# Kernel tuning notes

Hardware: AMD Instinct MI355X
Metric: run time of the kernel (lower is better)

## Reference

```python
import jax, jax.numpy as jnp
import numpy as np

B, CIN, H, W = 2, 8, 224, 224
P, S, K, WIN = 10, 5, 7, 3      # patchsize, stride, k neighbours, window radius = 15 // stride
E, F = 8, 64                    # embedding out-channels, cnn hidden features
N1 = (H - P) // S + 1
N2 = (W - P) // S + 1
N = N1 * N2                     # patches per image (43*43 = 1849)


def _conv(x, w, b):
    y = jax.lax.conv_general_dilated(x, w, (1, 1), 'SAME',
                                     dimension_numbers=('NCHW', 'OIHW', 'NCHW'))
    return y + b[None, :, None, None]


def _cnn3(x, w1, b1, w2, b2, w3, b3):
    # conv-relu, conv-relu, conv (depth=3, bn disabled)
    h = jax.nn.relu(_conv(x, w1, b1))
    h = jax.nn.relu(_conv(h, w2, b2))
    return _conv(h, w3, b3)


def _patches(x):
    # x: [B,C,H,W] -> [B, N, C*P*P] (im2col with stride S)
    ri = jnp.arange(N1)[:, None] * S + jnp.arange(P)[None, :]   # [N1,P]
    ci = jnp.arange(N2)[:, None] * S + jnp.arange(P)[None, :]   # [N2,P]
    p = x[:, :, ri, :][..., ci]            # [B,C,N1,P,N2,P]
    p = p.transpose(0, 2, 4, 1, 3, 5)      # [B,N1,N2,C,P,P]
    return p.reshape(x.shape[0], N, -1)


def _candidates():
    q1, q2 = jnp.meshgrid(jnp.arange(N1), jnp.arange(N2), indexing='ij')
    off = jnp.arange(-WIN, WIN + 1)
    c1 = jnp.clip(q1[..., None, None] + off[:, None], 0, N1 - 1)   # [N1,N2,7,7]
    c2 = jnp.clip(q2[..., None, None] + off[None, :], 0, N2 - 1)
    return (c1 * N2 + c2).reshape(N, -1)   # [N, m], m=49


def _fold(pats, C):
    # pats: [B,N,C*P*P] -> [B,C,H,W], overlap-add then normalize by counts
    pats = pats.reshape(B, N, C, P, P).transpose(0, 2, 1, 3, 4).reshape(B, C, -1)
    rr = jnp.arange(N1)[:, None] * S + jnp.arange(P)[None, :]
    cc = jnp.arange(N2)[:, None] * S + jnp.arange(P)[None, :]
    R = jnp.broadcast_to(rr[:, None, :, None], (N1, N2, P, P)).reshape(-1)
    Cc = jnp.broadcast_to(cc[None, :, None, :], (N1, N2, P, P)).reshape(-1)
    out = jnp.zeros((B, C, H, W), pats.dtype).at[:, :, R, Cc].add(pats)
    cnt = jnp.zeros((H, W), pats.dtype).at[R, Cc].add(1.0)
    return out / jnp.maximum(cnt, 1.0)


def setup_inputs() -> dict:
    key = jax.random.key(0)
    ks = jax.random.split(key, 8)
    sd = 0.05
    d = {"x": jax.random.normal(ks[0], (B, CIN, H, W), jnp.float32)}
    # embedding cnn: CIN->F->F->E
    d["w1e"] = jax.random.normal(ks[1], (F, CIN, 3, 3), jnp.float32) * sd
    d["b1e"] = jnp.zeros((F,), jnp.float32)
    d["w2e"] = jax.random.normal(ks[2], (F, F, 3, 3), jnp.float32) * sd
    d["b2e"] = jnp.zeros((F,), jnp.float32)
    d["w3e"] = jax.random.normal(ks[3], (E, F, 3, 3), jnp.float32) * sd
    d["b3e"] = jnp.zeros((E,), jnp.float32)
    # temperature cnn: CIN->F->F->1
    d["w1t"] = jax.random.normal(ks[4], (F, CIN, 3, 3), jnp.float32) * sd
    d["b1t"] = jnp.zeros((F,), jnp.float32)
    d["w2t"] = jax.random.normal(ks[5], (F, F, 3, 3), jnp.float32) * sd
    d["b2t"] = jnp.zeros((F,), jnp.float32)
    d["w3t"] = jax.random.normal(ks[6], (1, F, 3, 3), jnp.float32) * sd
    d["b3t"] = jnp.zeros((1,), jnp.float32)
    return d


def reference(x, w1e, b1e, w2e, b2e, w3e, b3e, w1t, b1t, w2t, b2t, w3t, b3t):
    xe = _cnn3(x, w1e, b1e, w2e, b2e, w3e, b3e)           # [B,E,H,W] patch embedding
    log_temp = _cnn3(x, w1t, b1t, w2t, b2t, w3t, b3t)     # [B,1,H,W] log temperature

    pe = _patches(xe)                                     # [B,N,E*P*P]
    yp = _patches(x)                                      # [B,N,CIN*P*P]
    lt = _patches(log_temp).mean(-1)                      # [B,N] per-patch log temp
    idx = _candidates()                                   # [N,m]

    # negative squared euclidean distance, gathered at window candidates
    sq = jnp.sum(pe * pe, -1)                             # [B,N]
    G = jnp.einsum('bnd,bmd->bnm', pe, pe)                # [B,N,N] patch Gram
    Dfull = -(sq[:, :, None] + sq[:, None, :] - 2.0 * G)
    Dc = Dfull[:, jnp.arange(N)[:, None], idx]            # [B,N,m]

    self_mask = (idx == jnp.arange(N)[:, None])[None]     # exclude_self=True
    logits = Dc * jnp.exp(-lt)[..., None]                 # temperature-scaled
    logits = jnp.where(self_mask, -1e9, logits)

    # continuous (neural) k-nearest-neighbour weights
    ws, cur = [], logits
    for _ in range(K):
        w = jax.nn.softmax(cur, axis=-1)
        ws.append(w)
        cur = cur + jnp.log1p(-jnp.minimum(w, 1.0 - 1e-6))
    Wk = jnp.stack(ws, axis=-1)                           # [B,N,m,K]

    yg = yp[:, idx]                                       # [B,N,m,dy] gathered neighbour patches
    nb = jnp.einsum('bnmk,bnmd->kbnd', Wk, yg)            # [K,B,N,dy]
    vols = [_fold(nb[j], CIN) for j in range(K)]
    return jnp.concatenate([x] + vols, axis=1)            # [B,(K+1)*CIN,H,W]
```

## Files before the change

kernel.cpp:

```cpp
#include <hip/hip_runtime.h>
#include <math.h>

namespace {
constexpr int B_ = 2, CIN = 8, H_ = 224, W_ = 224;
constexpr int K_ = 7;
constexpr int F_ = 64, E_ = 8;
constexpr int N1 = 43, N2 = 43, N_ = N1 * N2;
constexpr int M_ = 49;
constexpr int D_ = 800;
constexpr int HW = H_ * W_;

constexpr size_t FHW = (size_t)B_ * F_ * HW;
constexpr size_t OFF_H1E = 0;
constexpr size_t OFF_H1T = OFF_H1E + FHW;
constexpr size_t OFF_H2E = OFF_H1T + FHW;
constexpr size_t OFF_H2T = OFF_H2E + FHW;
constexpr size_t OFF_WK  = 0;
constexpr size_t OFF_XCL = OFF_H1T;
constexpr size_t OFF_XE  = OFF_H2T + FHW;
constexpr size_t OFF_LTM = OFF_XE + (size_t)B_ * E_ * HW;
constexpr size_t OFF_PE  = OFF_LTM + (size_t)B_ * HW;
constexpr size_t OFF_LT  = OFF_PE + (size_t)B_ * N_ * D_;
constexpr size_t OFF_SQ  = OFF_LT + (size_t)B_ * N_;
constexpr int WPREP_N = 294912;
constexpr int WPREP1_N = 12288;
constexpr int WPREP3_N = 9216;
constexpr int WPREP_TOT = WPREP_N + WPREP1_N + 2 * WPREP3_N;

__device__ __forceinline__ int clampi(int v, int lo, int hi) {
  return min(max(v, lo), hi);
}

__device__ __forceinline__ int xcd_swz(int x, int nwg) {
  int xcd = x & 7, idx = x >> 3;
  int q = nwg >> 3, r = nwg & 7;
  int base = (xcd < r) ? xcd * (q + 1) : r * (q + 1) + (xcd - r) * q;
  return base + idx;
}

__device__ __forceinline__ unsigned short bf16_rne(float v) {
  unsigned u = __float_as_uint(v);
  return (unsigned short)((u + 0x7FFFu + ((u >> 16) & 1u)) >> 16);
}

typedef __attribute__((ext_vector_type(8))) short short8;
typedef __attribute__((ext_vector_type(4))) float float4v;
typedef __attribute__((ext_vector_type(2))) float float2v;
typedef __attribute__((ext_vector_type(4))) unsigned short ushort4v;
}

__global__ __launch_bounds__(256) void wprep_k(
    const float* __restrict__ w_e, const float* __restrict__ w_t,
    const float* __restrict__ w1e, const float* __restrict__ w1t,
    const float* __restrict__ w3e, const float* __restrict__ w3t,
    unsigned short* __restrict__ whi, unsigned short* __restrict__ wlo,
    unsigned short* __restrict__ whi1, unsigned short* __restrict__ wlo1,
    unsigned short* __restrict__ whi3, unsigned short* __restrict__ wlo3) {
  int t = blockIdx.x * 256 + threadIdx.x;
  if (t >= WPREP_TOT) return;
  float v;
  unsigned short* dh;
  unsigned short* dl;
  int di;
  if (t < WPREP_N) {
    int j = t & 7;
    int lane = (t >> 3) & 63;
    int wv = (t >> 9) & 3;
    int t2 = t >> 11;
    int idx = t2 % 9;
    int t3 = t2 / 9;
    int kcb = t3 & 1;
    int br = t3 >> 1;
    const float* wgt = br ? w_t : w_e;
    int co = wv * 16 + (lane & 15);
    int ci = kcb * 32 + 8 * (lane >> 4) + j;
    v = wgt[((size_t)co * 64 + ci) * 9 + idx];
    dh = whi; dl = wlo; di = t;
  } else if (t < WPREP_N + WPREP1_N) {
    int t1 = t - WPREP_N;
    int j = t1 & 7;
    int lane = (t1 >> 3) & 63;
    int wv = (t1 >> 9) & 3;
    int t2 = t1 >> 11;
    int ky = t2 % 3;
    int br = t2 / 3;
    const float* wgt = br ? w1t : w1e;
    int co = wv * 16 + (lane & 15);
    int kx = lane >> 4;
    int ci = j;
    v = (kx < 3) ? wgt[(((size_t)co * 8 + ci) * 3 + ky) * 3 + kx] : 0.f;
    dh = whi1; dl = wlo1; di = t1;
  } else {
    int t3v = t - WPREP_N - WPREP1_N;
    int set = t3v / WPREP3_N;
    int rem = t3v - set * WPREP3_N;
    int j = rem & 7;
    int lane = (rem >> 3) & 63;
    int t2 = rem >> 9;
    int idx = t2 % 9;
    int kcb = t2 / 9;
    int co = lane & 15;
    int ci = kcb * 32 + 8 * (lane >> 4) + j;
    if (set == 0)
      v = (co < 8) ? w3e[((size_t)co * 64 + ci) * 9 + idx] : 0.f;
    else
      v = (co == 0) ? w3t[(size_t)ci * 9 + idx] : 0.f;
    dh = whi3; dl = wlo3; di = t3v;
  }
  unsigned u = __float_as_uint(v);
  unsigned short hi = (unsigned short)(u >> 16);
  float rem = v - __uint_as_float(u & 0xffff0000u);
  unsigned short lo = (unsigned short)(__float_as_uint(rem) >> 16);
  dh[di] = hi;
  dl[di] = lo;
}

__global__ __launch_bounds__(256) void conv1_k(
    const float* __restrict__ x,
    const unsigned short* __restrict__ whi1, const unsigned short* __restrict__ wlo1,
    const float* __restrict__ b_e, unsigned short* __restrict__ o_e,
    const float* __restrict__ b_t, unsigned short* __restrict__ o_t) {
  const int tile = blockIdx.x;
  const int b = blockIdx.z & 1;
  const int br = blockIdx.z >> 1;
  const float* bias = br ? b_t : b_e;
  unsigned short* out = br ? o_t : o_e;

  const int th0 = (tile / 14) * 16, tw0 = (tile % 14) * 16;
  const int tid = threadIdx.x;
  const int wv = tid >> 6, lane = tid & 63;
  const int q = lane >> 4, n = lane & 15;

  __shared__ unsigned short sT[342 * 20];

  const float* xB = x + (size_t)b * CIN * HW;
#pragma unroll
  for (int it = 0; it < 2; ++it) {
    int s = tid + 256 * it;
    if (s < 342) {
      int lr = s / 19, lc = s - lr * 19;
      int gh = th0 + lr - 1, gw = tw0 + lc - 1;
      short8 h8, l8;
#pragma unroll
      for (int ci = 0; ci < 8; ++ci) { h8[ci] = 0; l8[ci] = 0; }
      if (lc < 18 && gh >= 0 && gh < H_ && gw >= 0 && gw < W_) {
        const float* xp = xB + (size_t)gh * W_ + gw;
#pragma unroll
        for (int ci = 0; ci < 8; ++ci) {
          float v = xp[(size_t)ci * HW];
          unsigned u = __float_as_uint(v);
          float rem = v - __uint_as_float(u & 0xffff0000u);
          h8[ci] = (short)(u >> 16);
          l8[ci] = (short)(__float_as_uint(rem) >> 16);
        }
      }
      *(short8*)&sT[s * 20] = h8;
      *(short8*)&sT[s * 20 + 8] = l8;
    }
  }

  const short8* wh8 = (const short8*)whi1;
  const short8* wl8 = (const short8*)wlo1;
  short8 Ah[3], Al[3];
#pragma unroll
  for (int ky = 0; ky < 3; ++ky) {
    int ab = ((br * 3 + ky) * 4 + wv) * 64 + lane;
    Ah[ky] = wh8[ab];
    Al[ky] = wl8[ab];
  }

  float4v acc[16];
#pragma unroll
  for (int pr = 0; pr < 16; ++pr) acc[pr] = (float4v)0.f;

  __syncthreads();

#pragma unroll
  for (int r = 0; r < 18; ++r) {
    const unsigned short* p = &sT[(r * 19 + n + q) * 20];
    short8 Bh = *(const short8*)p;
    short8 Bl = *(const short8*)(p + 8);
#pragma unroll
    for (int ky = 0; ky < 3; ++ky) {
      const int pr = r - ky;
      if (pr >= 0 && pr < 16) {
        acc[pr] = __builtin_amdgcn_mfma_f32_16x16x32_bf16(Ah[ky], Bh, acc[pr], 0, 0, 0);
        acc[pr] = __builtin_amdgcn_mfma_f32_16x16x32_bf16(Al[ky], Bh, acc[pr], 0, 0, 0);
        acc[pr] = __builtin_amdgcn_mfma_f32_16x16x32_bf16(Ah[ky], Bl, acc[pr], 0, 0, 0);
      }
    }
  }

  float4v bv = *(const float4v*)&bias[wv * 16 + 4 * q];
#pragma unroll
  for (int pr = 0; pr < 16; ++pr) {
    ushort4v hv;
#pragma unroll
    for (int r = 0; r < 4; ++r)
      hv[r] = bf16_rne(fmaxf(acc[pr][r] + bv[r], 0.f));
    *(ushort4v*)&out[(((size_t)b * H_ + th0 + pr) * W_ + tw0 + n) * 64 + wv * 16 + 4 * q] = hv;
  }
}

__global__ __launch_bounds__(256) void conv2_mfma_k(
    const unsigned short* __restrict__ in_e, const unsigned short* __restrict__ in_t,
    const unsigned short* __restrict__ whi, const unsigned short* __restrict__ wlo,
    const float* __restrict__ b_e, const float* __restrict__ b_t,
    unsigned short* __restrict__ ehi, unsigned short* __restrict__ elo,
    unsigned short* __restrict__ thi, unsigned short* __restrict__ tlo) {
  constexpr int NLD = 12;
  const int tile = blockIdx.x;
  const int b = blockIdx.z & 1;
  const int br = blockIdx.z >> 1;
  const unsigned short* in = br ? in_t : in_e;
  const float* bias = br ? b_t : b_e;
  unsigned short* ohi = br ? thi : ehi;
  unsigned short* olo = br ? tlo : elo;

  const int th0 = (tile / 14) * 8, tw0 = (tile % 14) * 16;
  const int tid = threadIdx.x;
  const int wv = tid >> 6, lane = tid & 63;
  const int q = lane >> 4, n = lane & 15;

  __shared__ unsigned short sT[2 * 128 * 68];
  unsigned* sT32 = (unsigned*)sT;

  float4v acc[8];
#pragma unroll
  for (int pr = 0; pr < 8; ++pr) acc[pr] = (float4v)0.f;

  const unsigned short* inB = in + (size_t)b * HW * 64;
  const short8* whi8 = (const short8*)whi;
  const short8* wlo8 = (const short8*)wlo;

  int po[NLD];
  unsigned okm = 0;
#pragma unroll
  for (int j = 0; j < NLD; ++j) {
    int s = tid + 256 * j;
    int sp = s >> 4, cp = s & 15;
    int lr = sp / 18, lc = sp - lr * 18;
    int gh = th0 + lr - 1, gw = tw0 + lc - 1;
    bool ok = (s < 2880) && gh >= 0 && gh < H_ && gw >= 0 && gw < W_;
    po[j] = ok ? (gh * W_ + gw) * 64 + 2 * cp : 0;
    if (ok) okm |= (1u << j);
  }

  for (int kcb = 0; kcb < 2; ++kcb) {
    unsigned stg[NLD];
#pragma unroll
    for (int j = 0; j < NLD; ++j)
      stg[j] = *(const unsigned*)&inB[(size_t)po[j] + kcb * 32];

    __syncthreads();
#pragma unroll
    for (int j = 0; j < NLD; ++j) {
      int s = tid + 256 * j;
      if (s < 2880) {
        int sp = s >> 4, cp = s & 15;
        sT32[sp * 18 + cp] = ((okm >> j) & 1) ? stg[j] : 0u;
      }
    }
    __syncthreads();

    short8 Ah[9], Al[9];
    const int abase = (((br * 2 + kcb) * 9) * 4 + wv) * 64 + lane;
#pragma unroll
    for (int idx = 0; idx < 9; ++idx) {
      Ah[idx] = whi8[abase + idx * 256];
      Al[idx] = wlo8[abase + idx * 256];
    }

#pragma unroll
    for (int r = 0; r < 10; ++r) {
      short8 Bh[3];
#pragma unroll
      for (int kx = 0; kx < 3; ++kx)
        Bh[kx] = *(const short8*)&sT[(r * 18 + n + kx) * 36 + 8 * q];
#pragma unroll
      for (int ky = 0; ky < 3; ++ky) {
        const int pr = r - ky;
        if (pr >= 0 && pr < 8) {
#pragma unroll
          for (int kx = 0; kx < 3; ++kx) {
            const int idx = ky * 3 + kx;
            acc[pr] = __builtin_amdgcn_mfma_f32_16x16x32_bf16(Ah[idx], Bh[kx], acc[pr], 0, 0, 0);
            acc[pr] = __builtin_amdgcn_mfma_f32_16x16x32_bf16(Al[idx], Bh[kx], acc[pr], 0, 0, 0);
          }
        }
      }
    }
  }

  float4v bv = *(const float4v*)&bias[wv * 16 + 4 * q];
  unsigned short* sHi = (unsigned short*)sT;
  unsigned short* sLo = sHi + 128 * 68;
  __syncthreads();
#pragma unroll
  for (int pr = 0; pr < 8; ++pr) {
    int px = pr * 16 + n;
    ushort4v hv, lv;
#pragma unroll
    for (int r = 0; r < 4; ++r) {
      float v = fmaxf(acc[pr][r] + bv[r], 0.f);
      unsigned u = __float_as_uint(v);
      float rem = v - __uint_as_float(u & 0xffff0000u);
      hv[r] = (unsigned short)(u >> 16);
      lv[r] = (unsigned short)(__float_as_uint(rem) >> 16);
    }
    *(ushort4v*)&sHi[px * 68 + wv * 16 + 4 * q] = hv;
    *(ushort4v*)&sLo[px * 68 + wv * 16 + 4 * q] = lv;
  }
  __syncthreads();
#pragma unroll
  for (int i = 0; i < 4; ++i) {
    int f = tid + 256 * i;
    int px = f >> 3, c8 = f & 7;
    int h = th0 + (px >> 4), w = tw0 + (px & 15);
    size_t o = ((size_t)(b * H_ + h) * W_ + w) * 64 + c8 * 8;
    *(short8*)&ohi[o] = *(const short8*)&sHi[px * 68 + c8 * 8];
    *(short8*)&olo[o] = *(const short8*)&sLo[px * 68 + c8 * 8];
  }
}

__global__ __launch_bounds__(256) void conv3_mfma_k(
    const unsigned short* __restrict__ h2ehi, const unsigned short* __restrict__ h2elo,
    const unsigned short* __restrict__ h2thi, const unsigned short* __restrict__ h2tlo,
    const unsigned short* __restrict__ whi3, const unsigned short* __restrict__ wlo3,
    const float* __restrict__ b3e, const float* __restrict__ b3t,
    float* __restrict__ xe, float* __restrict__ ltm) {
  constexpr int NLD = 12;
  const int tile = blockIdx.x;
  const int b = blockIdx.z & 1;
  const int br = blockIdx.z >> 1;
  const unsigned short* ihi = (br ? h2thi : h2ehi) + (size_t)b * HW * 64;
  const unsigned short* ilo = (br ? h2tlo : h2elo) + (size_t)b * HW * 64;

  const int th0 = (tile / 14) * 8, tw0 = (tile % 14) * 16;
  const int tid = threadIdx.x;
  const int wv = tid >> 6, lane = tid & 63;
  const int q = lane >> 4, n = lane & 15;

  __shared__ unsigned short sT[180 * 72];
  unsigned* sT32 = (unsigned*)sT;

  int po[NLD];
  unsigned okm = 0;
#pragma unroll
  for (int j = 0; j < NLD; ++j) {
    int s = tid + 256 * j;
    int sp = s >> 4, cp = s & 15;
    int lr = sp / 18, lc = sp - lr * 18;
    int gh = th0 + lr - 1, gw = tw0 + lc - 1;
    bool ok = (s < 2880) && gh >= 0 && gh < H_ && gw >= 0 && gw < W_;
    po[j] = ok ? (gh * W_ + gw) * 64 + 2 * cp : 0;
    if (ok) okm |= (1u << j);
  }

  const short8* wh8 = (const short8*)whi3;
  const short8* wl8 = (const short8*)wlo3;
  const int brBase = br * 1152;

  float4v acc[2];
  acc[0] = (float4v)0.f;
  acc[1] = (float4v)0.f;

  for (int kcb = 0; kcb < 2; ++kcb) {
    unsigned sgh[NLD], sgl[NLD];
#pragma unroll
    for (int j = 0; j < NLD; ++j) {
      sgh[j] = *(const unsigned*)&ihi[(size_t)po[j] + kcb * 32];
      sgl[j] = *(const unsigned*)&ilo[(size_t)po[j] + kcb * 32];
    }
    __syncthreads();
#pragma unroll
    for (int j = 0; j < NLD; ++j) {
      int s = tid + 256 * j;
      if (s < 2880) {
        int sp = s >> 4, cp = s & 15;
        bool ok = (okm >> j) & 1;
        sT32[sp * 36 + cp] = ok ? sgh[j] : 0u;
        sT32[sp * 36 + 16 + cp] = ok ? sgl[j] : 0u;
      }
    }
    __syncthreads();

    short8 Ah[9], Al[9];
#pragma unroll
    for (int idx = 0; idx < 9; ++idx) {
      int fe = brBase + (kcb * 9 + idx) * 64 + lane;
      Ah[idx] = wh8[fe];
      Al[idx] = wl8[fe];
    }

#pragma unroll
    for (int r = 0; r < 4; ++r) {
      const int rr = 2 * wv + r;
      short8 Bh[3], Bl[3];
#pragma unroll
      for (int kx = 0; kx < 3; ++kx) {
        const unsigned short* p = &sT[(rr * 18 + n + kx) * 72 + 8 * q];
        Bh[kx] = *(const short8*)p;
        Bl[kx] = *(const short8*)(p + 32);
      }
#pragma unroll
      for (int ky = 0; ky < 3; ++ky) {
        const int pl = r - ky;
        if (pl >= 0 && pl < 2) {
#pragma unroll
          for (int kx = 0; kx < 3; ++kx) {
            const int idx = ky * 3 + kx;
            acc[pl] = __builtin_amdgcn_mfma_f32_16x16x32_bf16(Ah[idx], Bh[kx], acc[pl], 0, 0, 0);
            acc[pl] = __builtin_amdgcn_mfma_f32_16x16x32_bf16(Al[idx], Bh[kx], acc[pl], 0, 0, 0);
            acc[pl] = __builtin_amdgcn_mfma_f32_16x16x32_bf16(Ah[idx], Bl[kx], acc[pl], 0, 0, 0);
          }
        }
      }
    }
  }

  if (br == 0) {
    if (q < 2) {
      float4v bv = *(const float4v*)&b3e[4 * q];
#pragma unroll
      for (int pl = 0; pl < 2; ++pl) {
        int h = th0 + 2 * wv + pl;
#pragma unroll
        for (int r = 0; r < 4; ++r)
          xe[((size_t)(b * 8 + 4 * q + r) * H_ + h) * W_ + tw0 + n] = acc[pl][r] + bv[r];
      }
    }
  } else {
    if (q == 0) {
      float bt = b3t[0];
#pragma unroll
      for (int pl = 0; pl < 2; ++pl) {
        int h = th0 + 2 * wv + pl;
        ltm[(size_t)b * HW + h * W_ + tw0 + n] = acc[pl][0] + bt;
      }
    }
  }
}

__global__ __launch_bounds__(256) void xcl_k(const float* __restrict__ x,
                                             float* __restrict__ xcl) {
  int i = blockIdx.x * 256 + threadIdx.x;
  if (i >= B_ * HW) return;
  int b = i / HW, pix = i % HW;
  const float* xp = x + (size_t)b * CIN * HW + pix;
  float4v v0, v1;
#pragma unroll
  for (int c = 0; c < 4; ++c) v0[c] = xp[(size_t)c * HW];
#pragma unroll
  for (int c = 0; c < 4; ++c) v1[c] = xp[(size_t)(4 + c) * HW];
  *(float4v*)&xcl[(size_t)i * 8] = v0;
  *(float4v*)&xcl[(size_t)i * 8 + 4] = v1;
}

__global__ __launch_bounds__(256) void prep_k(const float* __restrict__ xe,
                                              const float* __restrict__ ltm,
                                              float* __restrict__ pe,
                                              float* __restrict__ lt,
                                              float* __restrict__ sq) {
  const int n = blockIdx.x, b = blockIdx.y;
  const int tid = threadIdx.x;
  const int wv = tid >> 6, lane = tid & 63;
  const int q1 = n / N2, q2 = n % N2;
  const int r0 = q1 * 5, c0 = q2 * 5;

  float s = 0.f;
  float* peR = pe + ((size_t)b * N_ + n) * D_;
#pragma unroll
  for (int j = 0; j < 4; ++j) {
    int d = tid + 256 * j;
    if (d < D_) {
      int c = d / 100;
      int rr = (d / 10) % 10;
      int cc = d % 10;
      size_t si = ((size_t)(b * 8 + c) * H_ + r0 + rr) * W_ + c0 + cc;
      float ve = xe[si];
      peR[d] = ve;
      s += ve * ve;
    }
  }
  float t = 0.f;
  if (tid < 100) t = ltm[(size_t)b * HW + (r0 + tid / 10) * W_ + c0 + tid % 10];

#pragma unroll
  for (int off = 32; off > 0; off >>= 1) {
    s += __shfl_xor(s, off);
    t += __shfl_xor(t, off);
  }
  __shared__ float rs[4], rt[4];
  if (lane == 0) { rs[wv] = s; rt[wv] = t; }
  __syncthreads();
  if (tid == 0) {
    sq[b * N_ + n] = rs[0] + rs[1] + rs[2] + rs[3];
    lt[b * N_ + n] = (rt[0] + rt[1] + rt[2] + rt[3]) * 0.01f;
  }
}

__global__ __launch_bounds__(256) void attn_w_k(const float* __restrict__ pe,
                                                const float* __restrict__ lt,
                                                const float* __restrict__ sq,
                                                float* __restrict__ wk) {
  const int wv = threadIdx.x >> 6, lane = threadIdx.x & 63;
  const int ng = xcd_swz(blockIdx.x, (N_ + 3) / 4);
  const int n = ng * 4 + wv;
  if (n >= N_) return;
  const int b = blockIdx.y;
  const int q1 = n / N2, q2 = n % N2;

  const float* peB = pe + (size_t)b * N_ * D_;
  const float* qrow = peB + (size_t)n * D_;
  float q[13];
#pragma unroll
  for (int t = 0; t < 13; ++t) {
    int s = t * 64 + lane;
    q[t] = (s < D_) ? qrow[s] : 0.f;
  }

  const float sqn = sq[b * N_ + n];
  const float itemp = expf(-lt[b * N_ + n]);
  float gm = -INFINITY;

  for (int o1 = 0; o1 < 7; ++o1) {
    int c1 = clampi(q1 + o1 - 3, 0, N1 - 1);
    const float* rowb = peB + (size_t)(c1 * N2) * D_;
#pragma unroll
    for (int o2 = 0; o2 < 7; ++o2) {
      int c2 = clampi(q2 + o2 - 3, 0, N2 - 1);
      int cn = c1 * N2 + c2;
      const float* crow = rowb + (size_t)c2 * D_;
      float a = 0.f;
#pragma unroll
      for (int t = 0; t < 13; ++t) {
        float v;
        if (t < 12) v = crow[t * 64 + lane];
        else v = (lane < 32) ? crow[768 + lane] : 0.f;
        a += q[t] * v;
      }
#pragma unroll
      for (int off = 32; off > 0; off >>= 1) a += __shfl_xor(a, off);
      float Dv = -(sqn + sq[b * N_ + cn] - 2.f * a);
      float lg = (cn == n) ? -1e9f : Dv * itemp;
      const int m = o1 * 7 + o2;
      gm = (lane == m) ? lg : gm;
    }
  }

  float cur = (lane < M_) ? gm : -INFINITY;
  float* wrow = wk + (size_t)(b * N_ + n) * (M_ * K_);
#pragma unroll
  for (int k = 0; k < K_; ++k) {
    float mx = cur;
#pragma unroll
    for (int off = 32; off > 0; off >>= 1) mx = fmaxf(mx, __shfl_xor(mx, off));
    float e = (lane < M_) ? expf(cur - mx) : 0.f;
    float ssum = e;
#pragma unroll
    for (int off = 32; off > 0; off >>= 1) ssum += __shfl_xor(ssum, off);
    float w = e / ssum;
    if (lane < M_) wrow[lane * K_ + k] = w;
    cur += log1pf(-fminf(w, 1.f - 1e-6f));
  }
}

__global__ __launch_bounds__(256) void foldpv_k(const float* __restrict__ xcl,
                                                const float* __restrict__ wk,
                                                float* __restrict__ out) {
  const int tile = xcd_swz(blockIdx.x, 196);
  const int b = blockIdx.y;
  const int c0 = blockIdx.z * 4;
  const int t1 = tile / 14, t2 = tile % 14;
  const int ty0 = t1 * 16, tx0 = t2 * 16;
  const int tid = threadIdx.x;
  const int h = ty0 + (tid >> 4), w = tx0 + (tid & 15);
  const bool fast = (t1 >= 2 && t1 <= 11 && t2 >= 2 && t2 <= 11);

  __shared__ float smem[25 * 392];

  const float* xclB = xcl + (size_t)b * HW * 8;
  const int pix = h * W_ + w;
  float* outB = out + (size_t)b * 64 * HW + pix;

  {
    float4v pv = *(const float4v*)&xclB[(size_t)pix * 8 + c0];
#pragma unroll
    for (int c = 0; c < 4; ++c) outB[(size_t)(c0 + c) * HW] = pv[c];
  }

  float acc[4][7];
#pragma unroll
  for (int c = 0; c < 4; ++c)
#pragma unroll
    for (int k = 0; k < 7; ++k) acc[c][k] = 0.f;

  if (fast) {
    const int cl1_0 = (ty0 - 5) / 5, cl2_0 = (tx0 - 5) / 5;
    for (int s = tid; s < 16 * 392; s += 256) {
      int cell = s / 392, r = s - cell * 392;
      int m = r >> 3, k = r & 7;
      float v = 0.f;
      if (k < 7) {
        int q1c = cl1_0 + (cell >> 2), q2c = cl2_0 + (cell & 3);
        size_t base = (size_t)(b * N_ + q1c * N2 + q2c) * (M_ * K_) + m * 7 + k;
        v = 0.25f * (wk[base] + wk[base + M_ * K_] +
                     wk[base + (size_t)N2 * (M_ * K_)] +
                     wk[base + (size_t)(N2 + 1) * (M_ * K_)]);
      }
      smem[s] = v;
    }
    __syncthreads();

    const int cl1 = (h - 5) / 5 - cl1_0, cl2 = (w - 5) / 5 - cl2_0;
    const float* sSp = smem + (cl1 * 4 + cl2) * 392;
    int roff[7], coff[7];
#pragma unroll
    for (int o = 0; o < 7; ++o) {
      roff[o] = (h + 5 * (o - 3)) * W_;
      coff[o] = w + 5 * (o - 3);
    }
#pragma unroll
    for (int o1 = 0; o1 < 7; ++o1) {
#pragma unroll
      for (int o2 = 0; o2 < 7; ++o2) {
        float4v xv = *(const float4v*)&xclB[((size_t)(roff[o1] + coff[o2])) * 8 + c0];
        const float* sp = sSp + (o1 * 7 + o2) * 8;
        float4v w4 = *(const float4v*)sp;
        float2v w2 = *(const float2v*)(sp + 4);
        float w6 = sp[6];
#pragma unroll
        for (int c = 0; c < 4; ++c) {
          acc[c][0] += w4[0] * xv[c];
          acc[c][1] += w4[1] * xv[c];
          acc[c][2] += w4[2] * xv[c];
          acc[c][3] += w4[3] * xv[c];
          acc[c][4] += w2[0] * xv[c];
          acc[c][5] += w2[1] * xv[c];
          acc[c][6] += w6 * xv[c];
        }
      }
    }
#pragma unroll
    for (int k = 0; k < 7; ++k)
#pragma unroll
      for (int c = 0; c < 4; ++c)
        outB[(size_t)(8 + k * 8 + c0 + c) * HW] = acc[c][k];
    return;
  }

  const int q1lo_t = max(0, (ty0 - 5) / 5), q1hi_t = min(N1 - 1, (ty0 + 15) / 5);
  const int q2lo_t = max(0, (tx0 - 5) / 5), q2hi_t = min(N2 - 1, (tx0 + 15) / 5);
  const int nq1 = q1hi_t - q1lo_t + 1, nq2 = q2hi_t - q2lo_t + 1;

  {
    const int tot = nq1 * nq2 * 392;
    for (int s = tid; s < tot; s += 256) {
      int lq = s / 392, r = s - lq * 392;
      int m = r >> 3, k = r & 7;
      int n = (q1lo_t + lq / nq2) * N2 + (q2lo_t + lq % nq2);
      smem[s] = (k < 7) ? wk[(size_t)(b * N_ + n) * (M_ * K_) + m * 7 + k] : 0.f;
    }
  }
  __syncthreads();

  const int q1lo = max(0, (h - 5) / 5), q1hi = min(N1 - 1, h / 5);
  const int q2lo = max(0, (w - 5) / 5), q2hi = min(N2 - 1, w / 5);

  int cnt = 0;
  for (int q1 = q1lo; q1 <= q1hi; ++q1) {
    const int ib = h - 5 * q1;
    const int lq1 = q1 - q1lo_t;
    for (int q2 = q2lo; q2 <= q2hi; ++q2) {
      ++cnt;
      const int jb = w - 5 * q2;
      const float* wq = smem + (lq1 * nq2 + (q2 - q2lo_t)) * 392;
#pragma unroll
      for (int o1 = 0; o1 < 7; ++o1) {
        const int c1 = clampi(q1 + o1 - 3, 0, N1 - 1);
        const int row = c1 * 5 + ib;
#pragma unroll
        for (int o2 = 0; o2 < 7; ++o2) {
          const int c2 = clampi(q2 + o2 - 3, 0, N2 - 1);
          const int col = c2 * 5 + jb;
          float4v xv = *(const float4v*)&xclB[((size_t)row * W_ + col) * 8 + c0];
          const float* wp = wq + (o1 * 7 + o2) * 8;
          float4v w4 = *(const float4v*)wp;
          float2v w2 = *(const float2v*)(wp + 4);
          float w6 = wp[6];
#pragma unroll
          for (int c = 0; c < 4; ++c) {
            acc[c][0] += w4[0] * xv[c];
            acc[c][1] += w4[1] * xv[c];
            acc[c][2] += w4[2] * xv[c];
            acc[c][3] += w4[3] * xv[c];
            acc[c][4] += w2[0] * xv[c];
            acc[c][5] += w2[1] * xv[c];
            acc[c][6] += w6 * xv[c];
          }
        }
      }
    }
  }

  const float inv = (cnt > 0) ? 1.f / (float)cnt : 0.f;
#pragma unroll
  for (int k = 0; k < 7; ++k)
#pragma unroll
    for (int c = 0; c < 4; ++c)
      outB[(size_t)(8 + k * 8 + c0 + c) * HW] = acc[c][k] * inv;
}

extern "C" void kernel_launch(void* const* d_in, const int* in_sizes, int n_in,
                              void* d_out, int out_size, void* d_ws,
                              size_t ws_size, hipStream_t stream) {
  const float* x   = (const float*)d_in[0];
  const float* w1e = (const float*)d_in[1];
  const float* b1e = (const float*)d_in[2];
  const float* w2e = (const float*)d_in[3];
  const float* b2e = (const float*)d_in[4];
  const float* w3e = (const float*)d_in[5];
  const float* b3e = (const float*)d_in[6];
  const float* w1t = (const float*)d_in[7];
  const float* b1t = (const float*)d_in[8];
  const float* w2t = (const float*)d_in[9];
  const float* b2t = (const float*)d_in[10];
  const float* w3t = (const float*)d_in[11];
  const float* b3t = (const float*)d_in[12];

  float* ws  = (float*)d_ws;
  float* out = (float*)d_out;

  unsigned short* h1e = (unsigned short*)(ws + OFF_H1E);
  unsigned short* h1t = (unsigned short*)(ws + OFF_H1T);
  unsigned short* h2ehi = (unsigned short*)(ws + OFF_H2E);
  unsigned short* h2elo = h2ehi + (size_t)B_ * HW * 64;
  unsigned short* h2thi = (unsigned short*)(ws + OFF_H2T);
  unsigned short* h2tlo = h2thi + (size_t)B_ * HW * 64;
  float* wkb = ws + OFF_WK;
  float* xe  = ws + OFF_XE;
  float* ltm = ws + OFF_LTM;
  float* pe  = ws + OFF_PE;
  float* lt  = ws + OFF_LT;
  float* sqv = ws + OFF_SQ;
  unsigned short* whi  = (unsigned short*)(ws + OFF_XE);
  unsigned short* wlo  = whi + WPREP_N;
  unsigned short* whi1 = wlo + WPREP_N;
  unsigned short* wlo1 = whi1 + WPREP1_N;
  unsigned short* whi3 = (unsigned short*)(ws + OFF_PE);
  unsigned short* wlo3 = whi3 + 2 * WPREP3_N;
  float* xcl = ws + OFF_XCL;

  wprep_k<<<(WPREP_TOT + 255) / 256, 256, 0, stream>>>(
      w2e, w2t, w1e, w1t, w3e, w3t, whi, wlo, whi1, wlo1, whi3, wlo3);
  conv1_k<<<dim3(196, 1, 4), 256, 0, stream>>>(x, whi1, wlo1, b1e, h1e, b1t, h1t);
  conv2_mfma_k<<<dim3(392, 1, 4), 256, 0, stream>>>(h1e, h1t, whi, wlo, b2e, b2t,
                                                    h2ehi, h2elo, h2thi, h2tlo);
  xcl_k<<<(B_ * HW + 255) / 256, 256, 0, stream>>>(x, xcl);
  conv3_mfma_k<<<dim3(392, 1, 4), 256, 0, stream>>>(h2ehi, h2elo, h2thi, h2tlo,
                                                    whi3, wlo3, b3e, b3t, xe, ltm);
  prep_k<<<dim3(N_, B_), 256, 0, stream>>>(xe, ltm, pe, lt, sqv);
  attn_w_k<<<dim3((N_ + 3) / 4, B_), 256, 0, stream>>>(pe, lt, sqv, wkb);
  foldpv_k<<<dim3(196, B_, 2), 256, 0, stream>>>(xcl, wkb, out);
}
```

Before: 275.2 us.

## Precompute averaged fold weights in a separate kernel and split fold channels finer

Adds a savg_k kernel that computes the 2x2 averaged neighbour weights once per cell into workspace, so each fold block loads precomputed values instead of recomputing four-way averages per tile. The fold kernel now handles 2 channels per block instead of 4 and launches twice as many blocks, aiming for more parallelism and lower register pressure. In exchange it adds a kernel launch and an extra write and read of the averaged weights. Each block also now rereads the shared weights and neighbour patches for half as many channels.

```diff
diff --git a/kernel.cpp b/kernel.cpp
--- a/kernel.cpp
+++ b/kernel.cpp
@@ -26,6 +26,7 @@
 constexpr int WPREP1_N = 12288;
 constexpr int WPREP3_N = 9216;
 constexpr int WPREP_TOT = WPREP_N + WPREP1_N + 2 * WPREP3_N;
+constexpr int SAVG_N = B_ * 42 * 42 * 392;
 
 __device__ __forceinline__ int clampi(int v, int lo, int hi) {
   return min(max(v, lo), hi);
@@ -566,12 +567,34 @@
   }
 }
 
+__global__ __launch_bounds__(256) void savg_k(const float* __restrict__ wk,
+                                              float* __restrict__ savg) {
+  int i = blockIdx.x * 256 + threadIdx.x;
+  if (i >= SAVG_N) return;
+  int r = i % 392;
+  int t = i / 392;
+  int cl2 = t % 42;
+  int t2 = t / 42;
+  int cl1 = t2 % 42;
+  int b = t2 / 42;
+  int m = r >> 3, k = r & 7;
+  float v = 0.f;
+  if (k < 7) {
+    size_t base = (size_t)(b * N_ + cl1 * N2 + cl2) * (M_ * K_) + m * 7 + k;
+    v = 0.25f * (wk[base] + wk[base + M_ * K_] +
+                 wk[base + (size_t)N2 * (M_ * K_)] +
+                 wk[base + (size_t)(N2 + 1) * (M_ * K_)]);
+  }
+  savg[i] = v;
+}
+
 __global__ __launch_bounds__(256) void foldpv_k(const float* __restrict__ xcl,
                                                 const float* __restrict__ wk,
+                                                const float* __restrict__ savg,
                                                 float* __restrict__ out) {
   const int tile = xcd_swz(blockIdx.x, 196);
   const int b = blockIdx.y;
-  const int c0 = blockIdx.z * 4;
+  const int c0 = blockIdx.z * 2;
   const int t1 = tile / 14, t2 = tile % 14;
   const int ty0 = t1 * 16, tx0 = t2 * 16;
   const int tid = threadIdx.x;
@@ -585,31 +608,24 @@
   float* outB = out + (size_t)b * 64 * HW + pix;
 
   {
-    float4v pv = *(const float4v*)&xclB[(size_t)pix * 8 + c0];
-#pragma unroll
-    for (int c = 0; c < 4; ++c) outB[(size_t)(c0 + c) * HW] = pv[c];
-  }
-
-  float acc[4][7];
-#pragma unroll
-  for (int c = 0; c < 4; ++c)
+    float2v pv = *(const float2v*)&xclB[(size_t)pix * 8 + c0];
+    outB[(size_t)c0 * HW] = pv[0];
+    outB[(size_t)(c0 + 1) * HW] = pv[1];
+  }
+
+  float acc[2][7];
+#pragma unroll
+  for (int c = 0; c < 2; ++c)
 #pragma unroll
     for (int k = 0; k < 7; ++k) acc[c][k] = 0.f;
 
   if (fast) {
     const int cl1_0 = (ty0 - 5) / 5, cl2_0 = (tx0 - 5) / 5;
+    const float* sb = savg + (size_t)b * 42 * 42 * 392;
     for (int s = tid; s < 16 * 392; s += 256) {
       int cell = s / 392, r = s - cell * 392;
-      int m = r >> 3, k = r & 7;
-      float v = 0.f;
-      if (k < 7) {
-        int q1c = cl1_0 + (cell >> 2), q2c = cl2_0 + (cell & 3);
-        size_t base = (size_t)(b * N_ + q1c * N2 + q2c) * (M_ * K_) + m * 7 + k;
-        v = 0.25f * (wk[base] + wk[base + M_ * K_] +
-                     wk[base + (size_t)N2 * (M_ * K_)] +
-                     wk[base + (size_t)(N2 + 1) * (M_ * K_)]);
-      }
-      smem[s] = v;
+      int q1c = cl1_0 + (cell >> 2), q2c = cl2_0 + (cell & 3);
+      smem[s] = sb[((size_t)q1c * 42 + q2c) * 392 + r];
     }
     __syncthreads();
 
@@ -625,13 +641,13 @@
     for (int o1 = 0; o1 < 7; ++o1) {
 #pragma unroll
       for (int o2 = 0; o2 < 7; ++o2) {
-        float4v xv = *(const float4v*)&xclB[((size_t)(roff[o1] + coff[o2])) * 8 + c0];
+        float2v xv = *(const float2v*)&xclB[((size_t)(roff[o1] + coff[o2])) * 8 + c0];
         const float* sp = sSp + (o1 * 7 + o2) * 8;
         float4v w4 = *(const float4v*)sp;
         float2v w2 = *(const float2v*)(sp + 4);
         float w6 = sp[6];
 #pragma unroll
-        for (int c = 0; c < 4; ++c) {
+        for (int c = 0; c < 2; ++c) {
           acc[c][0] += w4[0] * xv[c];
           acc[c][1] += w4[1] * xv[c];
           acc[c][2] += w4[2] * xv[c];
@@ -645,7 +661,7 @@
 #pragma unroll
     for (int k = 0; k < 7; ++k)
 #pragma unroll
-      for (int c = 0; c < 4; ++c)
+      for (int c = 0; c < 2; ++c)
         outB[(size_t)(8 + k * 8 + c0 + c) * HW] = acc[c][k];
     return;
   }
@@ -684,13 +700,13 @@
         for (int o2 = 0; o2 < 7; ++o2) {
           const int c2 = clampi(q2 + o2 - 3, 0, N2 - 1);
           const int col = c2 * 5 + jb;
-          float4v xv = *(const float4v*)&xclB[((size_t)row * W_ + col) * 8 + c0];
+          float2v xv = *(const float2v*)&xclB[((size_t)row * W_ + col) * 8 + c0];
           const float* wp = wq + (o1 * 7 + o2) * 8;
           float4v w4 = *(const float4v*)wp;
           float2v w2 = *(const float2v*)(wp + 4);
           float w6 = wp[6];
 #pragma unroll
-          for (int c = 0; c < 4; ++c) {
+          for (int c = 0; c < 2; ++c) {
             acc[c][0] += w4[0] * xv[c];
             acc[c][1] += w4[1] * xv[c];
             acc[c][2] += w4[2] * xv[c];
@@ -708,7 +724,7 @@
 #pragma unroll
   for (int k = 0; k < 7; ++k)
 #pragma unroll
-    for (int c = 0; c < 4; ++c)
+    for (int c = 0; c < 2; ++c)
       outB[(size_t)(8 + k * 8 + c0 + c) * HW] = acc[c][k] * inv;
 }
 
@@ -750,7 +766,8 @@
   unsigned short* wlo1 = whi1 + WPREP1_N;
   unsigned short* whi3 = (unsigned short*)(ws + OFF_PE);
   unsigned short* wlo3 = whi3 + 2 * WPREP3_N;
-  float* xcl = ws + OFF_XCL;
+  float* xcl  = ws + OFF_XCL;
+  float* savg = ws + OFF_PE;
 
   wprep_k<<<(WPREP_TOT + 255) / 256, 256, 0, stream>>>(
       w2e, w2t, w1e, w1t, w3e, w3t, whi, wlo, whi1, wlo1, whi3, wlo3);
@@ -762,5 +779,6 @@
                                                     whi3, wlo3, b3e, b3t, xe, ltm);
   prep_k<<<dim3(N_, B_), 256, 0, stream>>>(xe, ltm, pe, lt, sqv);
   attn_w_k<<<dim3((N_ + 3) / 4, B_), 256, 0, stream>>>(pe, lt, sqv, wkb);
-  foldpv_k<<<dim3(196, B_, 2), 256, 0, stream>>>(xcl, wkb, out);
-}
+  savg_k<<<(SAVG_N + 255) / 256, 256, 0, stream>>>(wkb, savg);
+  foldpv_k<<<dim3(196, B_, 4), 256, 0, stream>>>(xcl, wkb, savg, out);
+}
```

New measurement: 284.8 us. +3.5%, slower.
